# Kernel tuning notes

Hardware: AMD Instinct MI355X
Metric: run time of the kernel (lower is better)

## Reference

```python
import jax, jax.numpy as jnp
import numpy as np

G = 251            # grid_size = int(1e6 ** 0.4)
ORDER = 3          # KAN_SPLINE_ORDER
NB = G + ORDER     # num_basis = 254
H = (1.05 - (-0.05)) / G
# grid: [-order .. G+order] * h + lo  -> length G + 2*ORDER + 1 = 258 (same for every feature)
GRID = jnp.arange(-ORDER, G + ORDER + 1, dtype=jnp.float32) * H + (-0.05)
EPS = 1e-8


def bsplines(x):
    # x: [B, in] -> bases: [B, in, NB] via Cox-de Boor recursion
    x = x[..., None]
    b = ((x >= GRID[:-1]) & (x < GRID[1:])).astype(x.dtype)
    for k in range(1, ORDER + 1):
        left = (x - GRID[:-(k + 1)]) / jnp.maximum(GRID[k:-1] - GRID[:-(k + 1)], EPS)
        right = (GRID[k + 1:] - x) / jnp.maximum(GRID[k + 1:] - GRID[1:-k], EPS)
        b = left * b[..., :-1] + right * b[..., 1:]
    return b


def kan_layer(x, bw, sw, wb, ws, residual):
    # base path: SiLU then linear
    base = jax.nn.silu(x) @ bw.T                      # [B, out]
    # spline path: basis [B, in*NB] @ spline_weight.reshape(out, in*NB).T
    bas = bsplines(x).reshape(x.shape[0], -1)
    spl = bas @ sw.reshape(sw.shape[0], -1).T         # [B, out]
    out = wb * base + ws * spl
    return out + x if residual else out


def setup_inputs() -> dict:
    key = jax.random.key(0)
    ks = jax.random.split(key, 20)
    B, D, W = 2048, 64, 256
    d = {"x": jax.random.uniform(ks[0], (B, D), dtype=jnp.float32)}
    dims = [(W, D), (W, W), (W, W), (1, W)]
    for i, (o, inp) in enumerate(dims):
        d[f"bw{i}"] = jax.random.normal(ks[1 + 4 * i], (o, inp), dtype=jnp.float32) * 0.05
        d[f"sw{i}"] = jax.random.normal(ks[2 + 4 * i], (o, inp, NB), dtype=jnp.float32) * (0.5 / G)
        d[f"wb{i}"] = jnp.ones((1,), jnp.float32)
        d[f"ws{i}"] = jnp.ones((1,), jnp.float32)
    return d


def reference(x, bw0, sw0, wb0, ws0, bw1, sw1, wb1, ws1, bw2, sw2, wb2, ws2, bw3, sw3, wb3, ws3):
    h = kan_layer(x, bw0, sw0, wb0, ws0, False)   # input layer, no residual (64 -> 256)
    h = kan_layer(h, bw1, sw1, wb1, ws1, True)    # hidden, residual (256 -> 256)
    h = kan_layer(h, bw2, sw2, wb2, ws2, True)    # hidden, residual (256 -> 256)
    return kan_layer(h, bw3, sw3, wb3, ws3, False)  # output layer (256 -> 1)
```

## Files before the change

### kernel.cpp

```cpp
#include <hip/hip_runtime.h>

#define BATCH 2048
#define NB 254

typedef float f4u __attribute__((ext_vector_type(4), aligned(4)));

__device__ __forceinline__ float selw(int pd, float w0, float w1, float w2, float w3) {
    return (pd == 0) ? w0 : (pd == 1) ? w1 : (pd == 2) ? w2 : (pd == 3) ? w3 : 0.f;
}

__global__ __launch_bounds__(256) void basis_kernel(
    const float* __restrict__ act, int IN,
    const float* __restrict__ wbp, const float* __restrict__ wsp,
    float* __restrict__ sbuf, float4* __restrict__ vbuf, int* __restrict__ jbuf)
{
    int idx = blockIdx.x * 256 + threadIdx.x;
    int total = BATCH * IN;
    if (idx >= total) return;
    int i = idx / BATCH;
    int b = idx - i * BATCH;

    float x = act[(size_t)b * IN + i];
    float wb = wbp[0], wsc = wsp[0];

    float sil = x / (1.f + __expf(-x));

    const float LO = -0.05f;
    const float INVH = 228.18181818181818f;
    float uf = (x - LO) * INVH;
    float fm = floorf(uf);
    float t = uf - fm;
    int M = (int)fm + 3;

    bool valid = (M >= 0) && (M <= 256);
    float wsv = valid ? wsc : 0.f;

    float omt = 1.f - t;
    float t2 = t * t, t3 = t2 * t;
    const float S = 1.f / 6.f;
    float w0 = omt * omt * omt * S * wsv;
    float w1 = (3.f * t3 - 6.f * t2 + 4.f) * S * wsv;
    float w2 = (-3.f * t3 + 3.f * t2 + 3.f * t + 1.f) * S * wsv;
    float w3 = t3 * S * wsv;

    int js = M - 3;
    js = js < 0 ? 0 : js;
    js = js > (NB - 4) ? (NB - 4) : js;
    if (!valid) js = 0;
    int d = js - (M - 3);

    float vp0 = selw(0 + d, w0, w1, w2, w3);
    float vp1 = selw(1 + d, w0, w1, w2, w3);
    float vp2 = selw(2 + d, w0, w1, w2, w3);
    float vp3 = selw(3 + d, w0, w1, w2, w3);

    sbuf[idx] = sil * wb;
    vbuf[idx] = make_float4(vp0, vp1, vp2, vp3);
    jbuf[idx] = js;
}

template<int IN, int OT, bool RES, int IG, int BT>
__global__ __launch_bounds__(BT * IG) void accum_kernel(
    const float* __restrict__ sbuf, const float4* __restrict__ vbuf,
    const int* __restrict__ jbuf, const float* __restrict__ bw,
    const float* __restrict__ sw, const float* __restrict__ resid,
    float* __restrict__ out, int OUTF)
{
    int bx = threadIdx.x;
    int g  = threadIdx.y;
    int b  = blockIdx.y * BT + bx;
    int o0 = blockIdx.x * OT;

    float acc[OT];
#pragma unroll
    for (int k = 0; k < OT; k++) acc[k] = 0.f;

    const size_t ostride = (size_t)IN * NB;
    const int CH = IN / IG;
    const int i0 = g * CH;

    for (int ii = 0; ii < CH; ii++) {
        int i = i0 + ii;
        float s = sbuf[i * BATCH + b];
        float4 v = vbuf[i * BATCH + b];
        int j = jbuf[i * BATCH + b];
        const float* p = sw + (size_t)(o0 * IN + i) * NB + j;
        const float* bq = bw + o0 * IN + i;
#pragma unroll
        for (int oo = 0; oo < OT; oo++) {
            f4u w = *(const f4u*)(p + (size_t)oo * ostride);
            float bwv = bq[oo * IN];
            acc[oo] += s * bwv + v.x * w[0] + v.y * w[1] + v.z * w[2] + v.w * w[3];
        }
    }

    __shared__ float lds[OT * (IG - 1) * BT];
    if (g > 0) {
#pragma unroll
        for (int oo = 0; oo < OT; oo++)
            lds[(oo * (IG - 1) + (g - 1)) * BT + bx] = acc[oo];
    }
    __syncthreads();
    if (g == 0) {
#pragma unroll
        for (int oo = 0; oo < OT; oo++) {
            float a = acc[oo];
            for (int gg = 1; gg < IG; gg++)
                a += lds[(oo * (IG - 1) + (gg - 1)) * BT + bx];
            float r = RES ? resid[(size_t)b * OUTF + o0 + oo] : 0.f;
            out[(size_t)b * OUTF + o0 + oo] = a + r;
        }
    }
}

__global__ __launch_bounds__(256) void out_kernel(
    const float* __restrict__ sbuf, const float4* __restrict__ vbuf,
    const int* __restrict__ jbuf, const float* __restrict__ bw,
    const float* __restrict__ sw, float* __restrict__ out)
{
    int tid = threadIdx.x;
    int bl = tid >> 6;
    int ig = tid & 63;
    int b = blockIdx.x * 4 + bl;

    float acc = 0.f;
    for (int ii = ig; ii < 256; ii += 64) {
        float s = sbuf[ii * BATCH + b];
        float4 v = vbuf[ii * BATCH + b];
        int j = jbuf[ii * BATCH + b];
        const float* p = sw + (size_t)ii * NB + j;
        acc += s * bw[ii] + v.x * p[0] + v.y * p[1] + v.z * p[2] + v.w * p[3];
    }
#pragma unroll
    for (int dlt = 32; dlt >= 1; dlt >>= 1) acc += __shfl_down(acc, dlt, 64);
    if (ig == 0) out[b] = acc;
}

extern "C" void kernel_launch(void* const* d_in, const int* in_sizes, int n_in,
                              void* d_out, int out_size, void* d_ws, size_t ws_size,
                              hipStream_t stream)
{
    const float* x   = (const float*)d_in[0];
    const float* bw0 = (const float*)d_in[1];
    const float* sw0 = (const float*)d_in[2];
    const float* wb0 = (const float*)d_in[3];
    const float* ws0 = (const float*)d_in[4];
    const float* bw1 = (const float*)d_in[5];
    const float* sw1 = (const float*)d_in[6];
    const float* wb1 = (const float*)d_in[7];
    const float* ws1 = (const float*)d_in[8];
    const float* bw2 = (const float*)d_in[9];
    const float* sw2 = (const float*)d_in[10];
    const float* wb2 = (const float*)d_in[11];
    const float* ws2 = (const float*)d_in[12];
    const float* bw3 = (const float*)d_in[13];
    const float* sw3 = (const float*)d_in[14];
    const float* wb3 = (const float*)d_in[15];
    const float* ws3 = (const float*)d_in[16];

    char* ws = (char*)d_ws;
    float4* vbuf = (float4*)(ws);
    float*  sbuf = (float*)(ws + 8  * 1024 * 1024);
    int*    jbuf = (int*)  (ws + 10 * 1024 * 1024);
    float*  hA   = (float*)(ws + 12 * 1024 * 1024);
    float*  hB   = (float*)(ws + 14 * 1024 * 1024);

    float* out = (float*)d_out;

    dim3 ablk(128, 8);
    dim3 agrd(32, 16);

    basis_kernel<<<(BATCH * 64 + 255) / 256, 256, 0, stream>>>(x, 64, wb0, ws0, sbuf, vbuf, jbuf);
    accum_kernel<64, 8, false, 8, 128><<<agrd, ablk, 0, stream>>>(sbuf, vbuf, jbuf, bw0, sw0, nullptr, hA, 256);

    basis_kernel<<<(BATCH * 256 + 255) / 256, 256, 0, stream>>>(hA, 256, wb1, ws1, sbuf, vbuf, jbuf);
    accum_kernel<256, 8, true, 8, 128><<<agrd, ablk, 0, stream>>>(sbuf, vbuf, jbuf, bw1, sw1, hA, hB, 256);

    basis_kernel<<<(BATCH * 256 + 255) / 256, 256, 0, stream>>>(hB, 256, wb2, ws2, sbuf, vbuf, jbuf);
    accum_kernel<256, 8, true, 8, 128><<<agrd, ablk, 0, stream>>>(sbuf, vbuf, jbuf, bw2, sw2, hB, hA, 256);

    basis_kernel<<<(BATCH * 256 + 255) / 256, 256, 0, stream>>>(hA, 256, wb3, ws3, sbuf, vbuf, jbuf);
    out_kernel<<<BATCH / 4, 256, 0, stream>>>(sbuf, vbuf, jbuf, bw3, sw3, out);
}
```

Measured before the change: 299.9 us.

## Pack scale/index buffers, store hidden activations feature-major, hoist weight loads

Merges the separate SiLU-scale and index buffers into a single float2 stream, so each accumulation step issues one fewer load. Hidden activations and residuals are now written in feature-major layout, so the next basis kernel reads them contiguously instead of with a stride. The per-output weight gathers are hoisted into a register array so they can all be in flight together, and the accum block is halved to 64 batch columns with twice as many blocks. This trades extra register pressure for more memory-level parallelism and coalesced access.

```diff
diff --git a/kernel.cpp b/kernel.cpp
--- a/kernel.cpp
+++ b/kernel.cpp
@@ -9,10 +9,11 @@
     return (pd == 0) ? w0 : (pd == 1) ? w1 : (pd == 2) ? w2 : (pd == 3) ? w3 : 0.f;
 }
 
+template<bool TR>
 __global__ __launch_bounds__(256) void basis_kernel(
     const float* __restrict__ act, int IN,
     const float* __restrict__ wbp, const float* __restrict__ wsp,
-    float* __restrict__ sbuf, float4* __restrict__ vbuf, int* __restrict__ jbuf)
+    float2* __restrict__ sjbuf, float4* __restrict__ vbuf)
 {
     int idx = blockIdx.x * 256 + threadIdx.x;
     int total = BATCH * IN;
@@ -20,7 +21,7 @@
     int i = idx / BATCH;
     int b = idx - i * BATCH;
 
-    float x = act[(size_t)b * IN + i];
+    float x = TR ? act[idx] : act[(size_t)b * IN + i];
     float wb = wbp[0], wsc = wsp[0];
 
     float sil = x / (1.f + __expf(-x));
@@ -54,17 +55,15 @@
     float vp2 = selw(2 + d, w0, w1, w2, w3);
     float vp3 = selw(3 + d, w0, w1, w2, w3);
 
-    sbuf[idx] = sil * wb;
+    sjbuf[idx] = make_float2(sil * wb, __int_as_float(js));
     vbuf[idx] = make_float4(vp0, vp1, vp2, vp3);
-    jbuf[idx] = js;
 }
 
 template<int IN, int OT, bool RES, int IG, int BT>
-__global__ __launch_bounds__(BT * IG) void accum_kernel(
-    const float* __restrict__ sbuf, const float4* __restrict__ vbuf,
-    const int* __restrict__ jbuf, const float* __restrict__ bw,
-    const float* __restrict__ sw, const float* __restrict__ resid,
-    float* __restrict__ out, int OUTF)
+__global__ __launch_bounds__(BT * IG) void accum_f32(
+    const float2* __restrict__ sjbuf, const float4* __restrict__ vbuf,
+    const float* __restrict__ bw, const float* __restrict__ sw,
+    const float* __restrict__ resid, float* __restrict__ out)
 {
     int bx = threadIdx.x;
     int g  = threadIdx.y;
@@ -81,16 +80,22 @@
 
     for (int ii = 0; ii < CH; ii++) {
         int i = i0 + ii;
-        float s = sbuf[i * BATCH + b];
+        float2 sj = sjbuf[i * BATCH + b];
         float4 v = vbuf[i * BATCH + b];
-        int j = jbuf[i * BATCH + b];
+        int j = __float_as_int(sj.y);
+        float s = sj.x;
         const float* p = sw + (size_t)(o0 * IN + i) * NB + j;
-        const float* bq = bw + o0 * IN + i;
+        const float* bq = bw + (size_t)o0 * IN + i;
+
+        f4u w[OT];
+#pragma unroll
+        for (int oo = 0; oo < OT; oo++)
+            w[oo] = *(const f4u*)(p + (size_t)oo * ostride);
+
 #pragma unroll
         for (int oo = 0; oo < OT; oo++) {
-            f4u w = *(const f4u*)(p + (size_t)oo * ostride);
             float bwv = bq[oo * IN];
-            acc[oo] += s * bwv + v.x * w[0] + v.y * w[1] + v.z * w[2] + v.w * w[3];
+            acc[oo] += s * bwv + v.x * w[oo][0] + v.y * w[oo][1] + v.z * w[oo][2] + v.w * w[oo][3];
         }
     }
 
@@ -107,16 +112,17 @@
             float a = acc[oo];
             for (int gg = 1; gg < IG; gg++)
                 a += lds[(oo * (IG - 1) + (gg - 1)) * BT + bx];
-            float r = RES ? resid[(size_t)b * OUTF + o0 + oo] : 0.f;
-            out[(size_t)b * OUTF + o0 + oo] = a + r;
+            size_t oidx = (size_t)(o0 + oo) * BATCH + b;
+            float r = RES ? resid[oidx] : 0.f;
+            out[oidx] = a + r;
         }
     }
 }
 
 __global__ __launch_bounds__(256) void out_kernel(
-    const float* __restrict__ sbuf, const float4* __restrict__ vbuf,
-    const int* __restrict__ jbuf, const float* __restrict__ bw,
-    const float* __restrict__ sw, float* __restrict__ out)
+    const float2* __restrict__ sjbuf, const float4* __restrict__ vbuf,
+    const float* __restrict__ bw, const float* __restrict__ sw,
+    float* __restrict__ out)
 {
     int tid = threadIdx.x;
     int bl = tid >> 6;
@@ -125,11 +131,11 @@
 
     float acc = 0.f;
     for (int ii = ig; ii < 256; ii += 64) {
-        float s = sbuf[ii * BATCH + b];
+        float2 sj = sjbuf[ii * BATCH + b];
         float4 v = vbuf[ii * BATCH + b];
-        int j = jbuf[ii * BATCH + b];
+        int j = __float_as_int(sj.y);
         const float* p = sw + (size_t)ii * NB + j;
-        acc += s * bw[ii] + v.x * p[0] + v.y * p[1] + v.z * p[2] + v.w * p[3];
+        acc += sj.x * bw[ii] + v.x * p[0] + v.y * p[1] + v.z * p[2] + v.w * p[3];
     }
 #pragma unroll
     for (int dlt = 32; dlt >= 1; dlt >>= 1) acc += __shfl_down(acc, dlt, 64);
@@ -159,26 +165,25 @@
     const float* ws3 = (const float*)d_in[16];
 
     char* ws = (char*)d_ws;
-    float4* vbuf = (float4*)(ws);
-    float*  sbuf = (float*)(ws + 8  * 1024 * 1024);
-    int*    jbuf = (int*)  (ws + 10 * 1024 * 1024);
-    float*  hA   = (float*)(ws + 12 * 1024 * 1024);
-    float*  hB   = (float*)(ws + 14 * 1024 * 1024);
+    float4* vbuf  = (float4*)(ws);
+    float2* sjbuf = (float2*)(ws + 8  * 1024 * 1024);
+    float*  hA    = (float*)(ws + 12 * 1024 * 1024);
+    float*  hB    = (float*)(ws + 14 * 1024 * 1024);
 
     float* out = (float*)d_out;
 
-    dim3 ablk(128, 8);
-    dim3 agrd(32, 16);
+    dim3 ablk(64, 8);
+    dim3 agrd(32, 32);
 
-    basis_kernel<<<(BATCH * 64 + 255) / 256, 256, 0, stream>>>(x, 64, wb0, ws0, sbuf, vbuf, jbuf);
-    accum_kernel<64, 8, false, 8, 128><<<agrd, ablk, 0, stream>>>(sbuf, vbuf, jbuf, bw0, sw0, nullptr, hA, 256);
+    basis_kernel<false><<<(BATCH * 64 + 255) / 256, 256, 0, stream>>>(x, 64, wb0, ws0, sjbuf, vbuf);
+    accum_f32<64, 8, false, 8, 64><<<agrd, ablk, 0, stream>>>(sjbuf, vbuf, bw0, sw0, nullptr, hA);
 
-    basis_kernel<<<(BATCH * 256 + 255) / 256, 256, 0, stream>>>(hA, 256, wb1, ws1, sbuf, vbuf, jbuf);
-    accum_kernel<256, 8, true, 8, 128><<<agrd, ablk, 0, stream>>>(sbuf, vbuf, jbuf, bw1, sw1, hA, hB, 256);
+    basis_kernel<true><<<(BATCH * 256 + 255) / 256, 256, 0, stream>>>(hA, 256, wb1, ws1, sjbuf, vbuf);
+    accum_f32<256, 8, true, 8, 64><<<agrd, ablk, 0, stream>>>(sjbuf, vbuf, bw1, sw1, hA, hB);
 
-    basis_kernel<<<(BATCH * 256 + 255) / 256, 256, 0, stream>>>(hB, 256, wb2, ws2, sbuf, vbuf, jbuf);
-    accum_kernel<256, 8, true, 8, 128><<<agrd, ablk, 0, stream>>>(sbuf, vbuf, jbuf, bw2, sw2, hB, hA, 256);
+    basis_kernel<true><<<(BATCH * 256 + 255) / 256, 256, 0, stream>>>(hB, 256, wb2, ws2, sjbuf, vbuf);
+    accum_f32<256, 8, true, 8, 64><<<agrd, ablk, 0, stream>>>(sjbuf, vbuf, bw2, sw2, hB, hA);
 
-    basis_kernel<<<(BATCH * 256 + 255) / 256, 256, 0, stream>>>(hA, 256, wb3, ws3, sbuf, vbuf, jbuf);
-    out_kernel<<<BATCH / 4, 256, 0, stream>>>(sbuf, vbuf, jbuf, bw3, sw3, out);
+    basis_kernel<true><<<(BATCH * 256 + 255) / 256, 256, 0, stream>>>(hA, 256, wb3, ws3, sjbuf, vbuf);
+    out_kernel<<<BATCH / 4, 256, 0, stream>>>(sjbuf, vbuf, bw3, sw3, out);
 }
```

After: 295.2 us. Within noise of the previous version (-1.6%).
